# Kernel optimization log

Measured on AMD Instinct MI355X. Metric: run time of the kernel, lower is better.

Reference implementation:

```python
import jax, jax.numpy as jnp
import numpy as np

B, T, M = 256, 1460, 16
KLU = 0.9
PNAMES = ["dd", "f_thr", "sumax", "beta", "perc", "kf", "ki", "kb"]
PRANGES = {"dd": (0.0, 10.0), "f_thr": (10.0, 60.0), "sumax": (20.0, 700.0), "beta": (1.0, 6.0),
           "perc": (0.0, 1.0), "kf": (1.0, 20.0), "ki": (1.0, 100.0), "kb": (10.0, 1000.0)}
INIT_STATES = {"ss": 0.0, "sf": 1.0, "su": 5.0, "si": 10.0, "sb": 15.0}


def setup_inputs() -> dict:
    key = jax.random.key(0)
    k1, k2, k3, k4 = jax.random.split(key, 4)
    precip = jax.random.uniform(k1, (B, T)) * 10.0   # mm/day, nonnegative
    pet = jax.random.uniform(k2, (B, T)) * 5.0       # mm/day, nonnegative
    temp = jax.random.normal(k3, (B, T)) * 10.0      # deg C, mixed sign -> snow branch active
    x_conceptual = jnp.stack([precip, pet, temp], axis=-1).astype(jnp.float32)
    lstm_out = (jax.random.normal(k4, (B, T, len(PNAMES) * M)) * 0.5).astype(jnp.float32)
    return {"x_conceptual": x_conceptual, "lstm_out": lstm_out}


def _shm_forward(x_conceptual, lstm_out):
    Bs, Ts = x_conceptual.shape[0], x_conceptual.shape[1]
    lo = lstm_out.reshape(Bs, Ts, len(PNAMES), -1)  # [B,T,n_param,n_models]
    Ms = lo.shape[-1]
    # dynamic sigmoid-rescale parameter mapping
    params = {}
    for i, name in enumerate(PNAMES):
        lo_r, hi_r = PRANGES[name]
        params[name] = lo_r + jax.nn.sigmoid(lo[:, :, i, :]) * (hi_r - lo_r)

    prec = jnp.broadcast_to(x_conceptual[:, :, 0:1], (Bs, Ts, Ms))
    et = jnp.broadcast_to(x_conceptual[:, :, 1:2], (Bs, Ts, Ms))
    temp = jnp.broadcast_to(x_conceptual[:, :, 2:3], (Bs, Ts, Ms))
    frozen = temp < 0.0
    snow_melt = jnp.where(frozen, 0.0, temp * params["dd"])
    liquid_p = jnp.where(frozen, 0.0, prec)
    snow = jnp.where(frozen, prec, 0.0)
    pwp = 0.8 * params["sumax"]

    tm = lambda a: jnp.swapaxes(a, 0, 1)  # -> time-major [T,B,M]
    xs = (tm(snow_melt), tm(snow), tm(liquid_p), tm(et), tm(pwp),
          tm(params["f_thr"]), tm(params["sumax"]), tm(params["beta"]),
          tm(params["perc"]), tm(params["kf"]), tm(params["ki"]), tm(params["kb"]))
    init = tuple(jnp.full((Bs, Ms), v, dtype=x_conceptual.dtype) for v in INIT_STATES.values())

    def step(carry, x_t):
        ss, sf, su, si, sb = carry
        sm, sn, lp, e, pwp_t, f_thr, sumax, beta, perc, kf, ki, kb = x_t
        # snow bucket
        qs_out = jnp.minimum(ss, sm)
        ss = ss - qs_out + sn
        qsp_out = qs_out + lp
        # split into fast / unsaturated flow at threshold
        qf_in = jnp.maximum(0.0, qsp_out - f_thr)
        qu_in = jnp.minimum(qsp_out, f_thr)
        # fast reservoir
        sf = sf + qf_in
        qf_out = sf / kf
        sf = sf - qf_out
        # unsaturated zone
        psi = (su / sumax) ** beta
        su_temp = su + qu_in * (1.0 - psi)
        su = jnp.minimum(su_temp, sumax)
        qu_out = qu_in * psi + jnp.maximum(0.0, su_temp - sumax)
        ktetha = jnp.where(su <= pwp_t, su / sumax, 1.0)
        ret = e * KLU * ktetha
        su = jnp.maximum(0.0, su - ret)
        # interflow reservoir
        qi_in = qu_out * perc
        si = si + qi_in
        qi_out = si / ki
        si = si - qi_out
        # baseflow reservoir
        qb_in = qu_out * (1.0 - perc)
        sb = sb + qb_in
        qb_out = sb / kb
        sb = sb - qb_out
        q = jnp.mean(qf_out + qi_out + qb_out, axis=-1)  # mean over model entities
        return (ss, sf, su, si, sb), q

    _, q = jax.lax.scan(step, init, xs)
    y_hat = jnp.swapaxes(q, 0, 1)[:, :, None]  # [B,T,1]
    return y_hat


def reference(x_conceptual, lstm_out):
    return _shm_forward(x_conceptual, lstm_out)
```

## Files before the change

### kernel.cpp

```cpp
#include <hip/hip_runtime.h>
#include <hip/hip_fp16.h>
#include <stdint.h>

#define T_LEN 1460
#define NBT (256 * T_LEN)
#define NREC (NBT * 16)
#define CSZ 20
#define PCH (CSZ * 1024)
#define VCH (CSZ * 64)
#define Q1CH (CSZ * 512)
#define Q2CH (CSZ * 256)

typedef __attribute__((address_space(3))) char lds_c;
typedef __attribute__((address_space(1))) const char g_c;

__device__ __forceinline__ float sigmf(float x) {
    float e = __builtin_amdgcn_exp2f(-1.44269504f * x);
    return __builtin_amdgcn_rcpf(1.0f + e);
}
__device__ __forceinline__ float rcpf(float x) { return __builtin_amdgcn_rcpf(x); }

__device__ __forceinline__ uint32_t pkh2(float a, float b) {
    __half2 h = __floats2half2_rn(a, b);
    union { __half2 h; uint32_t u; } c; c.h = h; return c.u;
}
__device__ __forceinline__ float2 h2f(uint32_t u) {
    union { uint32_t u; __half2 h; } c; c.u = u;
    return __half22float2(c.h);
}

__device__ __forceinline__ float row_sum16(float x) {
    x += __int_as_float(__builtin_amdgcn_update_dpp(0, __float_as_int(x), 0xB1, 0xF, 0xF, true));
    x += __int_as_float(__builtin_amdgcn_update_dpp(0, __float_as_int(x), 0x4E, 0xF, 0xF, true));
    x += __int_as_float(__builtin_amdgcn_update_dpp(0, __float_as_int(x), 0x141, 0xF, 0xF, true));
    x += __int_as_float(__builtin_amdgcn_update_dpp(0, __float_as_int(x), 0x140, 0xF, 0xF, true));
    return x;
}

__global__ __launch_bounds__(256) void shm_param_kernel(
    const float* __restrict__ xc, const float* __restrict__ lo,
    uint4* __restrict__ R2, float* __restrict__ V)
{
    const int tid = blockIdx.x * 256 + threadIdx.x;
    const int m  = tid & 15;
    const int bt = tid >> 4;

    const float* lr = lo + (size_t)bt * 128 + m;
    const float r0 = lr[0],   r1 = lr[16],  r2 = lr[32],  r3 = lr[48];
    const float r4 = lr[64],  r5 = lr[80],  r6 = lr[96],  r7 = lr[112];

    const float* xp = xc + (size_t)bt * 3;
    const float prec = xp[0], pet = xp[1], temp = xp[2];
    const bool frozen = (temp < 0.f);
    const float tpos = frozen ? 0.f : temp;

    const float dd    = 10.f * sigmf(r0);
    const float sm    = tpos * dd;
    const float f_thr = fmaf(sigmf(r1), 50.f, 10.f);
    const float sumax = fmaf(sigmf(r2), 680.f, 20.f);
    const float beta  = fmaf(sigmf(r3), 5.f, 1.f);
    const float perc  = sigmf(r4);
    const float rkf   = rcpf(fmaf(sigmf(r5), 19.f, 1.f));
    const float rki   = rcpf(fmaf(sigmf(r6), 99.f, 1.f));
    const float rkb   = rcpf(fmaf(sigmf(r7), 990.f, 10.f));

    R2[tid] = make_uint4(pkh2(sm, f_thr), pkh2(sumax, beta),
                         pkh2(perc, rkf), pkh2(rki, rkb));
    if (m == 0)
        *(float4*)(V + (size_t)bt * 4) =
            make_float4(frozen ? prec : 0.f, frozen ? 0.f : prec, 0.9f * pet, 0.f);
}

__global__ __launch_bounds__(192, 1) void shm_serial_kernel(
    const char* __restrict__ R2,
    const char* __restrict__ V,
    float* __restrict__ out)
{
    __shared__ __align__(16) char pring[4 * PCH];
    __shared__ __align__(16) char vring[3 * VCH];
    __shared__ __align__(16) char q1[3 * Q1CH];
    __shared__ __align__(16) char q2[2 * Q2CH];

    const int lane = threadIdx.x & 63;
    const int wid  = threadIdx.x >> 6;
    const int m = lane & 15;
    const int bbase = blockIdx.x * 4;
    const int b = bbase + (lane >> 4);
    float* op = out + (size_t)b * T_LEN;

    lds_c* plp = (lds_c*)pring;
    lds_c* plv = (lds_c*)vring;
    const int voff = (lane >> 4) << 4;

    float ss = 0.f;
    float su = 5.f;
    float sf = 1.f, si = 10.f, sb = 15.f, qk = 0.f;

    const char* pRd2 = R2 + (size_t)b * T_LEN * 256 + m * 16;
    const char* pV1 = V + ((size_t)(bbase + (lane & 3)) * T_LEN + (lane >> 2)) * 16;
    const char* pV2 = V + ((size_t)(bbase + (lane & 3)) * T_LEN + 16 + (lane >> 2)) * 16;

#define FOR20(X) X(0) X(1) X(2) X(3) X(4) X(5) X(6) X(7) X(8) X(9) \
                 X(10) X(11) X(12) X(13) X(14) X(15) X(16) X(17) X(18) X(19)

#define ISSUECHUNK(wbp, wbv) {                                                \
    _Pragma("unroll") for (int J = 0; J < 20; ++J) {                          \
        __builtin_amdgcn_global_load_lds((g_c*)pRd2, plp + (wbp) + J * 1024, 16, 0, 0); \
        pRd2 += 256;                                                          \
    }                                                                         \
    __builtin_amdgcn_global_load_lds((g_c*)pV1, plv + (wbv), 16, 0, 0);       \
    if (lane < 16)                                                            \
        __builtin_amdgcn_global_load_lds((g_c*)pV2, plv + (wbv) + 1024, 16, 0, 0); \
    pV1 += 320; pV2 += 320; }

#define SSTEP(J) {                                                            \
    const uint32_t ux = *(const uint32_t*)(pring + sp0 + (J) * 1024 + lane * 16); \
    const float2 p0 = h2f(ux);                                 \
    const float2 snl = *(const float2*)(vring + sv0 + (J) * 64 + voff);       \
    const float qs_out = fminf(ss, p0.x);                                     \
    ss = (ss - qs_out) + snl.x;                                               \
    const float qsp = qs_out + snl.y;                                         \
    const float qf_ = fmaxf(0.f, qsp - p0.y);                                 \
    const float qu_ = fminf(qsp, p0.y);                                       \
    *(float2*)(q1 + sq10 + (J) * 512 + lane * 8) = make_float2(qf_, qu_); }

#define USTEP(J) {                                                            \
    const uint32_t uy = *(const uint32_t*)(pring + sp1 + (J) * 1024 + lane * 16 + 4); \
    const float2 p1 = h2f(uy);                               \
    const float et09 = *(const float*)(vring + sv1 + (J) * 64 + voff + 8);    \
    const float qu_in = *(const float*)(q1 + sq11 + (J) * 512 + lane * 8 + 4);\
    const float sumax = p1.x, beta = p1.y;                                    \
    const float inv = rcpf(sumax);                                            \
    const float pwp = 0.8f * sumax;                                           \
    const float e_i = et09 * inv;                                             \
    const float u = su * inv;                                                 \
    const float psi = __builtin_amdgcn_exp2f(beta * __builtin_amdgcn_logf(u));\
    const float su_t = fmaf(qu_in, 1.f - psi, su);                            \
    const float su2 = fminf(su_t, sumax);                                     \
    const float ovf = fmaxf(0.f, su_t - sumax);                               \
    const float qu_out = fmaf(qu_in, psi, ovf);                               \
    const float ret = (su2 <= pwp) ? su2 * e_i : et09;                        \
    su = fmaxf(0.f, su2 - ret);                                               \
    *(float*)(q2 + sq21 + (J) * 256 + lane * 4) = qu_out; }

#define LSTEP(J, tt) {                                                        \
    const uint2 ub = *(const uint2*)(pring + sp2 + (J) * 1024 + lane * 16 + 8); \
    const float2 p2 = h2f(ub.x);                               \
    const float2 p3 = h2f(ub.y);                                \
    const float qf_in = *(const float*)(q1 + sq12 + (J) * 512 + lane * 8);    \
    const float quo = *(const float*)(q2 + sq22 + (J) * 256 + lane * 4);      \
    sf += qf_in; const float qf_out = sf * p2.y; sf -= qf_out;                \
    const float qi_in = quo * p2.x;                                           \
    si += qi_in; const float qi_out = si * p3.x; si -= qi_out;                \
    sb += (quo - qi_in); const float qb_out = sb * p3.y; sb -= qb_out;        \
    const float q_ = row_sum16(qf_out + qi_out + qb_out) * 0.0625f;           \
    qk = (m == ((tt) & 15)) ? q_ : qk;                                        \
    if (((tt) & 15) == 15) op[((tt) & ~15) + m] = qk; }

    if (wid == 0) ISSUECHUNK(0, 0)
    __syncthreads();

    for (int r = 0; r <= 74; ++r) {
        if (wid == 0) {
            if (r <= 71) ISSUECHUNK(((uint32_t)((r + 1) & 3)) * PCH,
                                    ((uint32_t)((r + 1) % 3)) * VCH)
            if (r <= 72) {
                const uint32_t sp0  = (uint32_t)(r & 3) * PCH;
                const uint32_t sv0  = (uint32_t)(r % 3) * VCH;
                const uint32_t sq10 = (uint32_t)(r % 3) * Q1CH;
                FOR20(SSTEP)
            }
        } else if (wid == 1) {
            if (r >= 1 && r <= 73) {
                const int cu = r - 1;
                const uint32_t sp1  = (uint32_t)(cu & 3) * PCH;
                const uint32_t sv1  = (uint32_t)(cu % 3) * VCH;
                const uint32_t sq11 = (uint32_t)(cu % 3) * Q1CH;
                const uint32_t sq21 = (uint32_t)(cu & 1) * Q2CH;
                FOR20(USTEP)
            }
        } else {
            if (r >= 2) {
                const int cl = r - 2;
                const uint32_t sp2  = (uint32_t)(cl & 3) * PCH;
                const uint32_t sq12 = (uint32_t)(cl % 3) * Q1CH;
                const uint32_t sq22 = (uint32_t)(cl & 1) * Q2CH;
                const int t0 = CSZ * cl;
                LSTEP(0,  t0)      LSTEP(1,  t0 + 1)  LSTEP(2,  t0 + 2)
                LSTEP(3,  t0 + 3)  LSTEP(4,  t0 + 4)  LSTEP(5,  t0 + 5)
                LSTEP(6,  t0 + 6)  LSTEP(7,  t0 + 7)  LSTEP(8,  t0 + 8)
                LSTEP(9,  t0 + 9)  LSTEP(10, t0 + 10) LSTEP(11, t0 + 11)
                LSTEP(12, t0 + 12) LSTEP(13, t0 + 13) LSTEP(14, t0 + 14)
                LSTEP(15, t0 + 15) LSTEP(16, t0 + 16) LSTEP(17, t0 + 17)
                LSTEP(18, t0 + 18) LSTEP(19, t0 + 19)
            }
        }
        __syncthreads();
    }

    if (wid == 2 && m < 4) op[1456 + m] = qk;

#undef FOR20
#undef ISSUECHUNK
#undef SSTEP
#undef USTEP
#undef LSTEP
}

#define CS 10
#define NCHUNK 146
#define IST 66

__device__ __forceinline__ float lane0f(float x) {
    return __int_as_float(__builtin_amdgcn_readlane(__float_as_int(x), 0));
}

__global__ __launch_bounds__(256, 1) void shm_pc_kernel(
    const float* __restrict__ xc, const float* __restrict__ lo,
    float* __restrict__ out)
{
    __shared__ float pbuf[2][CS][8][IST];
    __shared__ float bbuf[2][CS][4][4];

    const int lane  = threadIdx.x & 63;
    const int wid   = threadIdx.x >> 6;
    const int bbase = blockIdx.x * 4;

    const int ip = lane >> 3;
    const float A  = (ip==1)?10.f : (ip==2)?20.f : (ip==3)?1.f :
                     (ip==5)?1.f  : (ip==6)?1.f  : (ip==7)?10.f : 0.f;
    const float Bc = (ip==0)?10.f : (ip==1)?50.f : (ip==2)?680.f : (ip==3)?5.f :
                     (ip==4)?1.f  : (ip==5)?19.f : (ip==6)?99.f  : 990.f;
    const bool drcp = (ip >= 5);
    const bool dsm  = (ip == 0);
    const int  mm   = (2*lane) & 15;

    auto produce = [&](int cc, int buf) {
        const int t0 = cc * CS;
        float2 raw[14];
        float xr0[14], xr1[14], xr2[14];
#pragma unroll
        for (int r = 0; r < 14; ++r) {
            const int tau = (wid - 1) + 3 * r;
            if (tau < 40) {
                const int g  = tau / CS;
                const int tl = tau - g * CS;
                const size_t rowoff = (size_t)(bbase + g) * T_LEN + (t0 + tl);
                raw[r] = *(const float2*)(lo + rowoff * 128 + 2 * lane);
                if (lane == 0) {
                    const float* xp = xc + rowoff * 3;
                    xr0[r] = xp[0]; xr1[r] = xp[1]; xr2[r] = xp[2];
                }
            }
        }
#pragma unroll
        for (int r = 0; r < 14; ++r) {
            const int tau = (wid - 1) + 3 * r;
            if (tau < 40) {
                const int g  = tau / CS;
                const int tl = tau - g * CS;
                const float prec = lane0f(xr0[r]);
                const float pet  = lane0f(xr1[r]);
                const float temp = lane0f(xr2[r]);
                const bool frozen = (temp < 0.f);
                const float tpos = frozen ? 0.f : temp;
                const float sn   = frozen ? prec : 0.f;
                const float lpq  = frozen ? 0.f : prec;
                const float et09 = 0.9f * pet;

                float v0 = fmaf(sigmf(raw[r].x), Bc, A);
                float v1 = fmaf(sigmf(raw[r].y), Bc, A);
                v0 = drcp ? rcpf(v0) : v0;
                v1 = drcp ? rcpf(v1) : v1;
                v0 = dsm ? v0 * tpos : v0;
                v1 = dsm ? v1 * tpos : v1;

                float* dst = &pbuf[buf][tl][ip][g * 16 + mm];
                *(float2*)dst = make_float2(v0, v1);
                if (lane == 0)
                    *(float4*)&bbuf[buf][tl][g][0] = make_float4(sn, lpq, et09, 0.f);
            }
        }
    };

    const int g = lane >> 4, m = lane & 15;
    float ss = 0.f, sf = 1.f, su = 5.f, si = 10.f, sb = 15.f;
    float* op = out + (size_t)(bbase + g) * T_LEN;

    if (wid != 0) produce(0, 0);
    __syncthreads();

    for (int c = 0; c < NCHUNK; ++c) {
        if (wid == 0) {
            const int buf = c & 1;
#pragma unroll
            for (int tl = 0; tl < CS; ++tl) {
                const float* rec = &pbuf[buf][tl][0][lane];
                const float sm    = rec[0 * IST];
                const float f_thr = rec[1 * IST];
                const float sumax = rec[2 * IST];
                const float beta  = rec[3 * IST];
                const float perc  = rec[4 * IST];
                const float rkf   = rec[5 * IST];
                const float rki   = rec[6 * IST];
                const float rkb   = rec[7 * IST];
                const float4 bx = *(const float4*)&bbuf[buf][tl][g][0];

                float qs_out = fminf(ss, sm);
                ss = ss - qs_out + bx.x;
                float qsp = qs_out + bx.y;
                float qf_in = fmaxf(0.f, qsp - f_thr);
                float qu_in = fminf(qsp, f_thr);
                sf += qf_in;
                float qf_out = sf * rkf;
                sf -= qf_out;
                float inv_sumax = rcpf(sumax);
                float u = su * inv_sumax;
                float psi = __builtin_amdgcn_exp2f(beta * __builtin_amdgcn_logf(u));
                float su_temp = fmaf(qu_in, 1.f - psi, su);
                su = fminf(su_temp, sumax);
                float ovf = fmaxf(0.f, su_temp - sumax);
                float qu_out = fmaf(qu_in, psi, ovf);
                float pwp = 0.8f * sumax;
                float ktheta = (su <= pwp) ? su * inv_sumax : 1.f;
                float ret = bx.z * ktheta;
                su = fmaxf(0.f, su - ret);
                float qi_in = qu_out * perc;
                si += qi_in;
                float qi_out = si * rki;
                si -= qi_out;
                float qb_in = qu_out - qi_in;
                sb += qb_in;
                float qb_out = sb * rkb;
                sb -= qb_out;

                float q = row_sum16(qf_out + qi_out + qb_out) * 0.0625f;
                if (m == 0) op[c * CS + tl] = q;
            }
        } else if (c + 1 < NCHUNK) {
            produce(c + 1, (c + 1) & 1);
        }
        __syncthreads();
    }
}

extern "C" void kernel_launch(void* const* d_in, const int* in_sizes, int n_in,
                              void* d_out, int out_size, void* d_ws, size_t ws_size,
                              hipStream_t stream) {
    const float* xc = (const float*)d_in[0];
    const float* lo = (const float*)d_in[1];
    float* out = (float*)d_out;

    const size_t R2_BYTES = (size_t)NREC * 16;
    const size_t V_BYTES  = (size_t)NBT * 16;

    if (ws_size >= R2_BYTES + V_BYTES) {
        uint4* R2 = (uint4*)d_ws;
        float* V  = (float*)((char*)d_ws + R2_BYTES);
        shm_param_kernel<<<dim3(NREC / 256), dim3(256), 0, stream>>>(xc, lo, R2, V);
        shm_serial_kernel<<<dim3(64), dim3(192), 0, stream>>>(
            (const char*)R2, (const char*)V, out);
    } else {
        shm_pc_kernel<<<dim3(64), dim3(256), 0, stream>>>(xc, lo, out);
    }
}
```

Baseline: 159.4 us.

## Split packed parameter records into planar arrays and hoist LDS loads in U-stage

The precomputed half-precision parameter records change from one interleaved 16-byte record per (b,t,m) to four planar 4-byte arrays. Each pipeline wave now reads a contiguous 4-byte-per-lane slice from LDS instead of a strided 16-byte record. The unsaturated-zone wave loads all 20 steps' inputs before running its serial chain, and the chain is rearranged to shorten the dependent path (su+qu_in precomputed, retention folded into a select of two precomputed candidates). The cost is four times as many 4-byte global_load_lds issues in the producer, in place of one 16-byte load per step.

```diff
diff --git a/kernel.cpp b/kernel.cpp
--- a/kernel.cpp
+++ b/kernel.cpp
@@ -39,7 +39,7 @@
 
 __global__ __launch_bounds__(256) void shm_param_kernel(
     const float* __restrict__ xc, const float* __restrict__ lo,
-    uint4* __restrict__ R2, float* __restrict__ V)
+    uint32_t* __restrict__ R2, float* __restrict__ V)
 {
     const int tid = blockIdx.x * 256 + threadIdx.x;
     const int m  = tid & 15;
@@ -64,8 +64,10 @@
     const float rki   = rcpf(fmaf(sigmf(r6), 99.f, 1.f));
     const float rkb   = rcpf(fmaf(sigmf(r7), 990.f, 10.f));
 
-    R2[tid] = make_uint4(pkh2(sm, f_thr), pkh2(sumax, beta),
-                         pkh2(perc, rkf), pkh2(rki, rkb));
+    R2[tid]            = pkh2(sm, f_thr);
+    R2[NREC + tid]     = pkh2(sumax, beta);
+    R2[2 * NREC + tid] = pkh2(perc, rkf);
+    R2[3 * NREC + tid] = pkh2(rki, rkb);
     if (m == 0)
         *(float4*)(V + (size_t)bt * 4) =
             make_float4(frozen ? prec : 0.f, frozen ? 0.f : prec, 0.9f * pet, 0.f);
@@ -96,7 +98,11 @@
     float su = 5.f;
     float sf = 1.f, si = 10.f, sb = 15.f, qk = 0.f;
 
-    const char* pRd2 = R2 + (size_t)b * T_LEN * 256 + m * 16;
+    const size_t boff = (((size_t)b * T_LEN) * 16 + m) * 4;
+    const char* pR0 = R2 + boff;
+    const char* pR1 = R2 + (size_t)NREC * 4 + boff;
+    const char* pR2p = R2 + (size_t)NREC * 8 + boff;
+    const char* pR3 = R2 + (size_t)NREC * 12 + boff;
     const char* pV1 = V + ((size_t)(bbase + (lane & 3)) * T_LEN + (lane >> 2)) * 16;
     const char* pV2 = V + ((size_t)(bbase + (lane & 3)) * T_LEN + 16 + (lane >> 2)) * 16;
 
@@ -105,17 +111,19 @@
 
 #define ISSUECHUNK(wbp, wbv) {                                                \
     _Pragma("unroll") for (int J = 0; J < 20; ++J) {                          \
-        __builtin_amdgcn_global_load_lds((g_c*)pRd2, plp + (wbp) + J * 1024, 16, 0, 0); \
-        pRd2 += 256;                                                          \
+        __builtin_amdgcn_global_load_lds((g_c*)(pR0 + J * 64),  plp + (wbp) + J * 1024,       4, 0, 0); \
+        __builtin_amdgcn_global_load_lds((g_c*)(pR1 + J * 64),  plp + (wbp) + J * 1024 + 256, 4, 0, 0); \
+        __builtin_amdgcn_global_load_lds((g_c*)(pR2p + J * 64), plp + (wbp) + J * 1024 + 512, 4, 0, 0); \
+        __builtin_amdgcn_global_load_lds((g_c*)(pR3 + J * 64),  plp + (wbp) + J * 1024 + 768, 4, 0, 0); \
     }                                                                         \
     __builtin_amdgcn_global_load_lds((g_c*)pV1, plv + (wbv), 16, 0, 0);       \
     if (lane < 16)                                                            \
         __builtin_amdgcn_global_load_lds((g_c*)pV2, plv + (wbv) + 1024, 16, 0, 0); \
+    pR0 += 1280; pR1 += 1280; pR2p += 1280; pR3 += 1280;                      \
     pV1 += 320; pV2 += 320; }
 
 #define SSTEP(J) {                                                            \
-    const uint32_t ux = *(const uint32_t*)(pring + sp0 + (J) * 1024 + lane * 16); \
-    const float2 p0 = h2f(ux);                                 \
+    const float2 p0 = h2f(*(const uint32_t*)(pring + sp0 + (J) * 1024 + lane * 4)); \
     const float2 snl = *(const float2*)(vring + sv0 + (J) * 64 + voff);       \
     const float qs_out = fminf(ss, p0.x);                                     \
     ss = (ss - qs_out) + snl.x;                                               \
@@ -124,29 +132,32 @@
     const float qu_ = fminf(qsp, p0.y);                                       \
     *(float2*)(q1 + sq10 + (J) * 512 + lane * 8) = make_float2(qf_, qu_); }
 
-#define USTEP(J) {                                                            \
-    const uint32_t uy = *(const uint32_t*)(pring + sp1 + (J) * 1024 + lane * 16 + 4); \
-    const float2 p1 = h2f(uy);                               \
-    const float et09 = *(const float*)(vring + sv1 + (J) * 64 + voff + 8);    \
-    const float qu_in = *(const float*)(q1 + sq11 + (J) * 512 + lane * 8 + 4);\
-    const float sumax = p1.x, beta = p1.y;                                    \
+#define ULOAD(J)                                                              \
+    const uint32_t UY##J = *(const uint32_t*)(pring + sp1 + (J) * 1024 + 256 + lane * 4); \
+    const float UE##J = *(const float*)(vring + sv1 + (J) * 64 + voff + 8);   \
+    const float UQ##J = *(const float*)(q1 + sq11 + (J) * 512 + lane * 8 + 4);
+
+#define UCHAIN(J) {                                                           \
+    const float2 p1 = h2f(UY##J);                            \
+    const float sumax = p1.x, beta = p1.y, et09 = UE##J, qu_in = UQ##J;       \
     const float inv = rcpf(sumax);                                            \
     const float pwp = 0.8f * sumax;                                           \
-    const float e_i = et09 * inv;                                             \
+    const float k1 = 1.f - et09 * inv;                                        \
+    const float spq = su + qu_in;                                             \
     const float u = su * inv;                                                 \
     const float psi = __builtin_amdgcn_exp2f(beta * __builtin_amdgcn_logf(u));\
-    const float su_t = fmaf(qu_in, 1.f - psi, su);                            \
+    const float su_t = fmaf(-qu_in, psi, spq);                                \
     const float su2 = fminf(su_t, sumax);                                     \
     const float ovf = fmaxf(0.f, su_t - sumax);                               \
     const float qu_out = fmaf(qu_in, psi, ovf);                               \
-    const float ret = (su2 <= pwp) ? su2 * e_i : et09;                        \
-    su = fmaxf(0.f, su2 - ret);                                               \
+    const float a_ = su2 * k1;                                                \
+    const float b_ = su2 - et09;                                              \
+    su = fmaxf(0.f, (su2 <= pwp) ? a_ : b_);                                  \
     *(float*)(q2 + sq21 + (J) * 256 + lane * 4) = qu_out; }
 
 #define LSTEP(J, tt) {                                                        \
-    const uint2 ub = *(const uint2*)(pring + sp2 + (J) * 1024 + lane * 16 + 8); \
-    const float2 p2 = h2f(ub.x);                               \
-    const float2 p3 = h2f(ub.y);                                \
+    const float2 p2 = h2f(*(const uint32_t*)(pring + sp2 + (J) * 1024 + 512 + lane * 4)); \
+    const float2 p3 = h2f(*(const uint32_t*)(pring + sp2 + (J) * 1024 + 768 + lane * 4)); \
     const float qf_in = *(const float*)(q1 + sq12 + (J) * 512 + lane * 8);    \
     const float quo = *(const float*)(q2 + sq22 + (J) * 256 + lane * 4);      \
     sf += qf_in; const float qf_out = sf * p2.y; sf -= qf_out;                \
@@ -177,7 +188,8 @@
                 const uint32_t sv1  = (uint32_t)(cu % 3) * VCH;
                 const uint32_t sq11 = (uint32_t)(cu % 3) * Q1CH;
                 const uint32_t sq21 = (uint32_t)(cu & 1) * Q2CH;
-                FOR20(USTEP)
+                FOR20(ULOAD)
+                FOR20(UCHAIN)
             }
         } else {
             if (r >= 2) {
@@ -203,7 +215,8 @@
 #undef FOR20
 #undef ISSUECHUNK
 #undef SSTEP
-#undef USTEP
+#undef ULOAD
+#undef UCHAIN
 #undef LSTEP
 }
 
@@ -355,8 +368,8 @@
     const size_t V_BYTES  = (size_t)NBT * 16;
 
     if (ws_size >= R2_BYTES + V_BYTES) {
-        uint4* R2 = (uint4*)d_ws;
-        float* V  = (float*)((char*)d_ws + R2_BYTES);
+        uint32_t* R2 = (uint32_t*)d_ws;
+        float* V = (float*)((char*)d_ws + R2_BYTES);
         shm_param_kernel<<<dim3(NREC / 256), dim3(256), 0, stream>>>(xc, lo, R2, V);
         shm_serial_kernel<<<dim3(64), dim3(192), 0, stream>>>(
             (const char*)R2, (const char*)V, out);
```

New measurement: 162.5 us. No clear change (+1.9%).
